# Kernel tuning notes

Measured on AMD Instinct MI355X. Metric: run time of the kernel, lower is better.

Reference implementation:

```python
import jax, jax.numpy as jnp
import numpy as np

EMBED_DIM = 768
NUM_HEADS = 12
HEAD_DIM = EMBED_DIM // NUM_HEADS


def setup_inputs() -> dict:
    key = jax.random.key(0)
    k1, k2, k3, k4, k5 = jax.random.split(key, 5)
    x = jax.random.normal(k1, (2, 4096, EMBED_DIM), dtype=jnp.float32)
    # nn.Linear(embedding_dim, 3*embedding_dim): weight [3d, d], bias [3d]
    w_qkv = jax.random.normal(k2, (3 * EMBED_DIM, EMBED_DIM), dtype=jnp.float32) * (1.0 / np.sqrt(EMBED_DIM))
    b_qkv = jax.random.normal(k3, (3 * EMBED_DIM,), dtype=jnp.float32) * 0.02
    # LayerNorm affine params
    ln_gamma = jnp.ones((EMBED_DIM,), dtype=jnp.float32)
    ln_beta = jnp.zeros((EMBED_DIM,), dtype=jnp.float32)
    return {"x": x, "w_qkv": w_qkv, "b_qkv": b_qkv, "ln_gamma": ln_gamma, "ln_beta": ln_beta}


def _layernorm(x, gamma, beta, eps=1e-5):
    mu = jnp.mean(x, axis=-1, keepdims=True)
    var = jnp.var(x, axis=-1, keepdims=True)
    return (x - mu) * jax.lax.rsqrt(var + eps) * gamma + beta


def reference(x, w_qkv, b_qkv, ln_gamma, ln_beta):
    b, n, d = x.shape
    h, hd = NUM_HEADS, HEAD_DIM
    qkv = x @ w_qkv.T + b_qkv                      # [b, n, 3d]
    qkv = qkv.reshape(b, n, 3, h, hd)
    qkv = jnp.transpose(qkv, (2, 0, 3, 1, 4))      # [3, b, h, n, hd]
    Q, K, V = qkv[0], qkv[1], qkv[2]
    scale = 1.0 / np.sqrt(hd).astype(np.float32)
    scores = jnp.einsum('bhqd,bhkd->bhqk', Q, K) * scale   # [b, h, n, n]
    attn = jax.nn.softmax(scores, axis=-1)
    out = jnp.einsum('bhqk,bhkd->bhqd', attn, V)           # [b, h, n, hd]
    out = jnp.transpose(out, (0, 2, 1, 3)).reshape(b, n, d)
    return _layernorm(x + out, ln_gamma, ln_beta)
```

## Files before the change

kernel.cpp:

```cpp
#include <hip/hip_runtime.h>
#include <stdint.h>

#define NUM_HEADS 12
#define HEAD_DIM 64
#define EMB 768
#define SEQ 4096
#define BATCH 2
#define ROWS (BATCH*SEQ)
#define DQKV (3*EMB)

typedef __attribute__((ext_vector_type(8))) __bf16 bf16x8;
typedef __attribute__((ext_vector_type(4))) float floatx4;

static __device__ __forceinline__ unsigned short f2bf(float f) {
  unsigned int u = __float_as_uint(f);
  u += 0x7FFFu + ((u >> 16) & 1u);
  return (unsigned short)(u >> 16);
}

static __device__ __forceinline__ unsigned int pack_bf2_trunc(float a, float b) {
  return __builtin_amdgcn_perm(__float_as_uint(b), __float_as_uint(a), 0x07060302u);
}

static __device__ __forceinline__ void async_cp16(void* lds, const void* g) {
  __builtin_amdgcn_global_load_lds(
      (__attribute__((address_space(1))) void*)(g),
      (__attribute__((address_space(3))) void*)(lds), 16, 0, 0);
}

__global__ __launch_bounds__(256) void cvt_bf16_kernel(
    const float* __restrict__ src, unsigned short* __restrict__ dst, int n4) {
  int i = blockIdx.x * blockDim.x + threadIdx.x;
  if (i >= n4) return;
  float4 v = ((const float4*)src)[i];
  ushort4 o;
  o.x = f2bf(v.x); o.y = f2bf(v.y); o.z = f2bf(v.z); o.w = f2bf(v.w);
  ((ushort4*)dst)[i] = o;
}

__global__ __launch_bounds__(256) void qkv_gemm_kernel(
    const unsigned short* __restrict__ xb, const unsigned short* __restrict__ wb,
    const float* __restrict__ bias,
    unsigned short* __restrict__ Qb, unsigned short* __restrict__ Kb,
    unsigned short* __restrict__ Vt) {
  __shared__ unsigned short As[128 * 64];
  __shared__ unsigned short Bs[128 * 64];
  const int t = threadIdx.x;
  const int lane = t & 63;
  const int w = t >> 6;
  const int wm = w >> 1, wn = w & 1;
  const int fr = lane & 15, fq = lane >> 4;
  const int fx = fr & 7;
  const int m0 = blockIdx.x * 128;
  const int n0 = blockIdx.y * 128;
  const int lr = t >> 3;
  const int sc = t & 7;

  floatx4 acc[4][4];
#pragma unroll
  for (int i = 0; i < 4; ++i)
#pragma unroll
    for (int j = 0; j < 4; ++j) acc[i][j] = (floatx4)(0.0f);

  for (int k0 = 0; k0 < EMB; k0 += 64) {
    __syncthreads();
#pragma unroll
    for (int i = 0; i < 4; ++i) {
      const int rr = i*32 + lr;
      const int cg = ((sc ^ (lr & 7)) * 8);
      async_cp16(&As[rr*64 + sc*8], &xb[(size_t)(m0 + rr)*EMB + k0 + cg]);
      async_cp16(&Bs[rr*64 + sc*8], &wb[(size_t)(n0 + rr)*EMB + k0 + cg]);
    }
    __syncthreads();
#pragma unroll
    for (int ks = 0; ks < 2; ++ks) {
      bf16x8 af[4], bfr[4];
#pragma unroll
      for (int i = 0; i < 4; ++i)
        af[i] = *(const bf16x8*)&As[(wm*64 + i*16 + fr)*64 + (((ks*4+fq) ^ fx)*8)];
#pragma unroll
      for (int j = 0; j < 4; ++j)
        bfr[j] = *(const bf16x8*)&Bs[(wn*64 + j*16 + fr)*64 + (((ks*4+fq) ^ fx)*8)];
#pragma unroll
      for (int i = 0; i < 4; ++i)
#pragma unroll
        for (int j = 0; j < 4; ++j)
          acc[i][j] = __builtin_amdgcn_mfma_f32_16x16x32_bf16(bfr[j], af[i], acc[i][j], 0, 0, 0);
    }
  }

  const int sel = n0 / EMB;
  const float qscale = 0.125f * 1.4426950408889634f;
  const float sc2 = (sel == 0) ? qscale : 1.0f;
#pragma unroll
  for (int i = 0; i < 4; ++i) {
    const int mr = m0 + wm*64 + i*16 + fr;
    const int b = mr / SEQ;
    const int nn = mr - b*SEQ;
#pragma unroll
    for (int j = 0; j < 4; ++j) {
      const int og = n0 + wn*64 + j*16 + fq*4;
      const int oo = og - sel*EMB;
      const int hh = oo >> 6, dd = oo & 63;
      const float4 bv = *(const float4*)&bias[og];
      if (sel == 2) {
        const size_t vtb = (((size_t)(b*NUM_HEADS + hh))*HEAD_DIM + dd)*SEQ + nn;
        Vt[vtb + 0*SEQ] = f2bf(acc[i][j][0] + bv.x);
        Vt[vtb + 1*SEQ] = f2bf(acc[i][j][1] + bv.y);
        Vt[vtb + 2*SEQ] = f2bf(acc[i][j][2] + bv.z);
        Vt[vtb + 3*SEQ] = f2bf(acc[i][j][3] + bv.w);
      } else {
        unsigned short* dst = (sel == 0) ? Qb : Kb;
        ushort4 pk;
        pk.x = f2bf((acc[i][j][0] + bv.x) * sc2);
        pk.y = f2bf((acc[i][j][1] + bv.y) * sc2);
        pk.z = f2bf((acc[i][j][2] + bv.z) * sc2);
        pk.w = f2bf((acc[i][j][3] + bv.w) * sc2);
        *(ushort4*)&dst[(((size_t)(b*NUM_HEADS + hh))*SEQ + nn)*HEAD_DIM + dd] = pk;
      }
    }
  }
}

__global__ __launch_bounds__(256, 3) void attn_kernel(
    const unsigned short* __restrict__ Qb, const unsigned short* __restrict__ Kb,
    const unsigned short* __restrict__ Vt, unsigned short* __restrict__ Oo) {
  __shared__ unsigned short Ks[128 * 64];
  __shared__ unsigned short Vs[64 * 128];
  const int t = threadIdx.x;
  const int lane = t & 63;
  const int w = t >> 6;
  const int fr = lane & 15, fq = lane >> 4;
  const int fx = fr & 7;
  const int bh = blockIdx.y;
  const int q0 = blockIdx.x * 128 + w * 32;

  bf16x8 aq[2][2];
#pragma unroll
  for (int g = 0; g < 2; ++g) {
    const size_t qoff = ((size_t)bh * SEQ + q0 + g*16 + fr) * HEAD_DIM;
    aq[g][0] = *(const bf16x8*)&Qb[qoff + fq*8];
    aq[g][1] = *(const bf16x8*)&Qb[qoff + 32 + fq*8];
  }

  union { unsigned int u[4]; bf16x8 b; } onesu;
  onesu.u[0] = onesu.u[1] = onesu.u[2] = onesu.u[3] = 0x3F803F80u;
  const bf16x8 onesb = onesu.b;

  floatx4 o[2][4];
  floatx4 lsum[2];
#pragma unroll
  for (int g = 0; g < 2; ++g) {
    lsum[g] = (floatx4)(0.f);
#pragma unroll
    for (int d = 0; d < 4; ++d) o[g][d] = (floatx4)(0.f);
  }

  const size_t kb = (size_t)bh * SEQ * HEAD_DIM;
  const size_t vb = (size_t)bh * HEAD_DIM * SEQ;

  for (int kc = 0; kc < SEQ; kc += 128) {
    __syncthreads();
#pragma unroll
    for (int i = 0; i < 4; ++i) {
      const int chunk = i*256 + t;
      const int r = chunk >> 3, c = chunk & 7;
      async_cp16(&Ks[chunk*8], &Kb[kb + (size_t)(kc + r)*HEAD_DIM + ((c ^ (r&7))*8)]);
    }
#pragma unroll
    for (int i = 0; i < 4; ++i) {
      const int chunk = i*256 + t;
      const int r = chunk >> 4, c = chunk & 15;
      async_cp16(&Vs[chunk*8], &Vt[vb + (size_t)r*SEQ + kc + ((c ^ (r&7))*8)]);
    }
    __syncthreads();

#pragma unroll
    for (int J = 0; J < 4; ++J) {
      floatx4 z[2][2];
#pragma unroll
      for (int jj = 0; jj < 2; ++jj) {
        const int row = (J*2 + jj)*16 + fr;
        bf16x8 k0 = *(const bf16x8*)&Ks[row*64 + ((fq ^ fx)*8)];
        bf16x8 k1 = *(const bf16x8*)&Ks[row*64 + (((fq+4) ^ fx)*8)];
#pragma unroll
        for (int g = 0; g < 2; ++g) {
          floatx4 accz = (floatx4)(0.f);
          accz = __builtin_amdgcn_mfma_f32_16x16x32_bf16(k0, aq[g][0], accz, 0, 0, 0);
          accz = __builtin_amdgcn_mfma_f32_16x16x32_bf16(k1, aq[g][1], accz, 0, 0, 0);
          z[g][jj] = accz;
        }
      }
      bf16x8 ap[2];
#pragma unroll
      for (int g = 0; g < 2; ++g) {
        float e0 = __builtin_amdgcn_exp2f(z[g][0][0]);
        float e1 = __builtin_amdgcn_exp2f(z[g][0][1]);
        float e2 = __builtin_amdgcn_exp2f(z[g][0][2]);
        float e3 = __builtin_amdgcn_exp2f(z[g][0][3]);
        float e4 = __builtin_amdgcn_exp2f(z[g][1][0]);
        float e5 = __builtin_amdgcn_exp2f(z[g][1][1]);
        float e6 = __builtin_amdgcn_exp2f(z[g][1][2]);
        float e7 = __builtin_amdgcn_exp2f(z[g][1][3]);
        union { unsigned int u[4]; bf16x8 b; } cv;
        cv.u[0] = pack_bf2_trunc(e0, e1);
        cv.u[1] = pack_bf2_trunc(e2, e3);
        cv.u[2] = pack_bf2_trunc(e4, e5);
        cv.u[3] = pack_bf2_trunc(e6, e7);
        ap[g] = cv.b;
      }
#pragma unroll
      for (int g = 0; g < 2; ++g)
        lsum[g] = __builtin_amdgcn_mfma_f32_16x16x32_bf16(ap[g], onesb, lsum[g], 0, 0, 0);
#pragma unroll
      for (int dt = 0; dt < 4; ++dt) {
        const int r = dt*16 + fr;
        const int c0 = 4*J + (fq >> 1);
        const int c1 = c0 + 2;
        union { ushort4 h[2]; bf16x8 b; } vv;
        vv.h[0] = *(const ushort4*)&Vs[r*128 + ((c0 ^ fx)*8) + (fq&1)*4];
        vv.h[1] = *(const ushort4*)&Vs[r*128 + ((c1 ^ fx)*8) + (fq&1)*4];
#pragma unroll
        for (int g = 0; g < 2; ++g)
          o[g][dt] = __builtin_amdgcn_mfma_f32_16x16x32_bf16(ap[g], vv.b, o[g][dt], 0, 0, 0);
      }
    }
  }

  const int b = bh / NUM_HEADS, hh = bh - b*NUM_HEADS;
#pragma unroll
  for (int g = 0; g < 2; ++g)
#pragma unroll
    for (int r4 = 0; r4 < 4; ++r4) {
      const float li = 1.0f / lsum[g][r4];
      const size_t obase = ((size_t)b*SEQ + q0 + g*16 + fq*4 + r4)*EMB + hh*HEAD_DIM;
#pragma unroll
      for (int dt = 0; dt < 4; ++dt)
        Oo[obase + dt*16 + fr] = f2bf(o[g][dt][r4] * li);
    }
}

__global__ __launch_bounds__(256) void ln_kernel(
    const float* __restrict__ x, const unsigned short* __restrict__ att,
    const float* __restrict__ gamma, const float* __restrict__ beta,
    float* __restrict__ out) {
  const int row = blockIdx.x;
  const size_t base = (size_t)row * EMB;
  const int t = threadIdx.x;
  float v[3];
  float s = 0.f, s2 = 0.f;
#pragma unroll
  for (int k = 0; k < 3; ++k) {
    const int c = t + k*256;
    float a = __uint_as_float(((unsigned int)att[base + c]) << 16);
    float val = x[base + c] + a;
    v[k] = val; s += val; s2 += val*val;
  }
#pragma unroll
  for (int off = 32; off > 0; off >>= 1) {
    s  += __shfl_down(s,  off);
    s2 += __shfl_down(s2, off);
  }
  __shared__ float red[8];
  if ((t & 63) == 0) { red[t >> 6] = s; red[4 + (t >> 6)] = s2; }
  __syncthreads();
  const float S  = red[0] + red[1] + red[2] + red[3];
  const float S2 = red[4] + red[5] + red[6] + red[7];
  const float mean = S * (1.0f / EMB);
  const float var  = S2 * (1.0f / EMB) - mean * mean;
  const float rstd = rsqrtf(var + 1e-5f);
#pragma unroll
  for (int k = 0; k < 3; ++k) {
    const int c = t + k*256;
    out[base + c] = (v[k] - mean) * rstd * gamma[c] + beta[c];
  }
}

extern "C" void kernel_launch(void* const* d_in, const int* in_sizes, int n_in,
                              void* d_out, int out_size, void* d_ws, size_t ws_size,
                              hipStream_t stream) {
  const float* x      = (const float*)d_in[0];
  const float* w_qkv  = (const float*)d_in[1];
  const float* b_qkv  = (const float*)d_in[2];
  const float* gamma  = (const float*)d_in[3];
  const float* beta   = (const float*)d_in[4];
  float* out = (float*)d_out;

  unsigned short* xb = (unsigned short*)d_ws;
  unsigned short* wb = xb + (size_t)ROWS * EMB;
  unsigned short* Qb = wb + (size_t)DQKV * EMB;
  unsigned short* Kb = Qb + (size_t)ROWS * EMB;
  unsigned short* Vt = Kb + (size_t)ROWS * EMB;
  unsigned short* att = Vt + (size_t)ROWS * EMB;

  cvt_bf16_kernel<<<(ROWS*EMB/4 + 255)/256, 256, 0, stream>>>(x, xb, ROWS*EMB/4);
  cvt_bf16_kernel<<<(DQKV*EMB/4 + 255)/256, 256, 0, stream>>>(w_qkv, wb, DQKV*EMB/4);
  qkv_gemm_kernel<<<dim3(ROWS/128, DQKV/128), 256, 0, stream>>>(xb, wb, b_qkv, Qb, Kb, Vt);
  attn_kernel<<<dim3(SEQ/128, BATCH*NUM_HEADS), 256, 0, stream>>>(Qb, Kb, Vt, att);
  ln_kernel<<<ROWS, 256, 0, stream>>>(x, att, gamma, beta, out);
}
```

Baseline: 258.6 us.

## Split V projection into transposed-output GEMM and widen attention blocks to 8 waves

The QKV GEMM is split into a Q/K kernel and a separate V kernel. The V kernel swaps the MFMA operands so each lane holds four consecutive sequence positions and can write the transposed V with packed 8-byte stores instead of scattered 2-byte stores. The attention kernel now uses 512 threads per block, with each wave handling 16 query rows instead of 32. This halves per-wave register use and the cooperative K/V tile load count per thread, at the cost of each K/V LDS read feeding half as many MFMAs and one extra kernel launch.

New measurement: 286.2 us. 1.11x slower.

```diff
diff --git a/kernel.cpp b/kernel.cpp
--- a/kernel.cpp
+++ b/kernel.cpp
@@ -38,11 +38,10 @@
   ((ushort4*)dst)[i] = o;
 }
 
-__global__ __launch_bounds__(256) void qkv_gemm_kernel(
+__global__ __launch_bounds__(256) void qk_gemm_kernel(
     const unsigned short* __restrict__ xb, const unsigned short* __restrict__ wb,
     const float* __restrict__ bias,
-    unsigned short* __restrict__ Qb, unsigned short* __restrict__ Kb,
-    unsigned short* __restrict__ Vt) {
+    unsigned short* __restrict__ Qb, unsigned short* __restrict__ Kb) {
   __shared__ unsigned short As[128 * 64];
   __shared__ unsigned short Bs[128 * 64];
   const int t = threadIdx.x;
@@ -92,6 +91,7 @@
   const int sel = n0 / EMB;
   const float qscale = 0.125f * 1.4426950408889634f;
   const float sc2 = (sel == 0) ? qscale : 1.0f;
+  unsigned short* dst = (sel == 0) ? Qb : Kb;
 #pragma unroll
   for (int i = 0; i < 4; ++i) {
     const int mr = m0 + wm*64 + i*16 + fr;
@@ -103,26 +103,87 @@
       const int oo = og - sel*EMB;
       const int hh = oo >> 6, dd = oo & 63;
       const float4 bv = *(const float4*)&bias[og];
-      if (sel == 2) {
-        const size_t vtb = (((size_t)(b*NUM_HEADS + hh))*HEAD_DIM + dd)*SEQ + nn;
-        Vt[vtb + 0*SEQ] = f2bf(acc[i][j][0] + bv.x);
-        Vt[vtb + 1*SEQ] = f2bf(acc[i][j][1] + bv.y);
-        Vt[vtb + 2*SEQ] = f2bf(acc[i][j][2] + bv.z);
-        Vt[vtb + 3*SEQ] = f2bf(acc[i][j][3] + bv.w);
-      } else {
-        unsigned short* dst = (sel == 0) ? Qb : Kb;
-        ushort4 pk;
-        pk.x = f2bf((acc[i][j][0] + bv.x) * sc2);
-        pk.y = f2bf((acc[i][j][1] + bv.y) * sc2);
-        pk.z = f2bf((acc[i][j][2] + bv.z) * sc2);
-        pk.w = f2bf((acc[i][j][3] + bv.w) * sc2);
-        *(ushort4*)&dst[(((size_t)(b*NUM_HEADS + hh))*SEQ + nn)*HEAD_DIM + dd] = pk;
-      }
-    }
-  }
-}
-
-__global__ __launch_bounds__(256, 3) void attn_kernel(
+      ushort4 pk;
+      pk.x = f2bf((acc[i][j][0] + bv.x) * sc2);
+      pk.y = f2bf((acc[i][j][1] + bv.y) * sc2);
+      pk.z = f2bf((acc[i][j][2] + bv.z) * sc2);
+      pk.w = f2bf((acc[i][j][3] + bv.w) * sc2);
+      *(ushort4*)&dst[(((size_t)(b*NUM_HEADS + hh))*SEQ + nn)*HEAD_DIM + dd] = pk;
+    }
+  }
+}
+
+__global__ __launch_bounds__(256) void v_gemm_kernel(
+    const unsigned short* __restrict__ xb, const unsigned short* __restrict__ wb,
+    const float* __restrict__ bias, unsigned short* __restrict__ Vt) {
+  __shared__ unsigned short As[128 * 64];
+  __shared__ unsigned short Bs[128 * 64];
+  const int t = threadIdx.x;
+  const int lane = t & 63;
+  const int w = t >> 6;
+  const int wm = w >> 1, wn = w & 1;
+  const int fr = lane & 15, fq = lane >> 4;
+  const int fx = fr & 7;
+  const int m0 = blockIdx.x * 128;
+  const int n0 = 2*EMB + blockIdx.y * 128;
+  const int lr = t >> 3;
+  const int sc = t & 7;
+
+  floatx4 acc[4][4];
+#pragma unroll
+  for (int i = 0; i < 4; ++i)
+#pragma unroll
+    for (int j = 0; j < 4; ++j) acc[i][j] = (floatx4)(0.0f);
+
+  for (int k0 = 0; k0 < EMB; k0 += 64) {
+    __syncthreads();
+#pragma unroll
+    for (int i = 0; i < 4; ++i) {
+      const int rr = i*32 + lr;
+      const int cg = ((sc ^ (lr & 7)) * 8);
+      async_cp16(&As[rr*64 + sc*8], &xb[(size_t)(m0 + rr)*EMB + k0 + cg]);
+      async_cp16(&Bs[rr*64 + sc*8], &wb[(size_t)(n0 + rr)*EMB + k0 + cg]);
+    }
+    __syncthreads();
+#pragma unroll
+    for (int ks = 0; ks < 2; ++ks) {
+      bf16x8 af[4], bfr[4];
+#pragma unroll
+      for (int i = 0; i < 4; ++i)
+        af[i] = *(const bf16x8*)&As[(wm*64 + i*16 + fr)*64 + (((ks*4+fq) ^ fx)*8)];
+#pragma unroll
+      for (int j = 0; j < 4; ++j)
+        bfr[j] = *(const bf16x8*)&Bs[(wn*64 + j*16 + fr)*64 + (((ks*4+fq) ^ fx)*8)];
+#pragma unroll
+      for (int i = 0; i < 4; ++i)
+#pragma unroll
+        for (int j = 0; j < 4; ++j)
+          acc[i][j] = __builtin_amdgcn_mfma_f32_16x16x32_bf16(af[i], bfr[j], acc[i][j], 0, 0, 0);
+    }
+  }
+
+#pragma unroll
+  for (int i = 0; i < 4; ++i) {
+    const int mr = m0 + wm*64 + i*16 + fq*4;
+    const int b = mr / SEQ;
+    const int nn = mr - b*SEQ;
+#pragma unroll
+    for (int j = 0; j < 4; ++j) {
+      const int feat = n0 + wn*64 + j*16 + fr;
+      const int oo = feat - 2*EMB;
+      const int hh = oo >> 6, dd = oo & 63;
+      const float bv = bias[feat];
+      ushort4 pk;
+      pk.x = f2bf(acc[i][j][0] + bv);
+      pk.y = f2bf(acc[i][j][1] + bv);
+      pk.z = f2bf(acc[i][j][2] + bv);
+      pk.w = f2bf(acc[i][j][3] + bv);
+      *(ushort4*)&Vt[(((size_t)(b*NUM_HEADS + hh))*HEAD_DIM + dd)*SEQ + nn] = pk;
+    }
+  }
+}
+
+__global__ __launch_bounds__(512, 6) void attn_kernel(
     const unsigned short* __restrict__ Qb, const unsigned short* __restrict__ Kb,
     const unsigned short* __restrict__ Vt, unsigned short* __restrict__ Oo) {
   __shared__ unsigned short Ks[128 * 64];
@@ -133,28 +194,20 @@
   const int fr = lane & 15, fq = lane >> 4;
   const int fx = fr & 7;
   const int bh = blockIdx.y;
-  const int q0 = blockIdx.x * 128 + w * 32;
-
-  bf16x8 aq[2][2];
-#pragma unroll
-  for (int g = 0; g < 2; ++g) {
-    const size_t qoff = ((size_t)bh * SEQ + q0 + g*16 + fr) * HEAD_DIM;
-    aq[g][0] = *(const bf16x8*)&Qb[qoff + fq*8];
-    aq[g][1] = *(const bf16x8*)&Qb[qoff + 32 + fq*8];
-  }
+  const int q0 = blockIdx.x * 128 + w * 16;
+
+  const size_t qoff = ((size_t)bh * SEQ + q0 + fr) * HEAD_DIM;
+  bf16x8 aq0 = *(const bf16x8*)&Qb[qoff + fq*8];
+  bf16x8 aq1 = *(const bf16x8*)&Qb[qoff + 32 + fq*8];
 
   union { unsigned int u[4]; bf16x8 b; } onesu;
   onesu.u[0] = onesu.u[1] = onesu.u[2] = onesu.u[3] = 0x3F803F80u;
   const bf16x8 onesb = onesu.b;
 
-  floatx4 o[2][4];
-  floatx4 lsum[2];
-#pragma unroll
-  for (int g = 0; g < 2; ++g) {
-    lsum[g] = (floatx4)(0.f);
-#pragma unroll
-    for (int d = 0; d < 4; ++d) o[g][d] = (floatx4)(0.f);
-  }
+  floatx4 o[4];
+  floatx4 lsum = (floatx4)(0.f);
+#pragma unroll
+  for (int d = 0; d < 4; ++d) o[d] = (floatx4)(0.f);
 
   const size_t kb = (size_t)bh * SEQ * HEAD_DIM;
   const size_t vb = (size_t)bh * HEAD_DIM * SEQ;
@@ -162,14 +215,14 @@
   for (int kc = 0; kc < SEQ; kc += 128) {
     __syncthreads();
 #pragma unroll
-    for (int i = 0; i < 4; ++i) {
-      const int chunk = i*256 + t;
+    for (int i = 0; i < 2; ++i) {
+      const int chunk = i*512 + t;
       const int r = chunk >> 3, c = chunk & 7;
       async_cp16(&Ks[chunk*8], &Kb[kb + (size_t)(kc + r)*HEAD_DIM + ((c ^ (r&7))*8)]);
     }
 #pragma unroll
-    for (int i = 0; i < 4; ++i) {
-      const int chunk = i*256 + t;
+    for (int i = 0; i < 2; ++i) {
+      const int chunk = i*512 + t;
       const int r = chunk >> 4, c = chunk & 15;
       async_cp16(&Vs[chunk*8], &Vt[vb + (size_t)r*SEQ + kc + ((c ^ (r&7))*8)]);
     }
@@ -177,41 +230,32 @@
 
 #pragma unroll
     for (int J = 0; J < 4; ++J) {
-      floatx4 z[2][2];
+      floatx4 z[2];
 #pragma unroll
       for (int jj = 0; jj < 2; ++jj) {
         const int row = (J*2 + jj)*16 + fr;
         bf16x8 k0 = *(const bf16x8*)&Ks[row*64 + ((fq ^ fx)*8)];
         bf16x8 k1 = *(const bf16x8*)&Ks[row*64 + (((fq+4) ^ fx)*8)];
-#pragma unroll
-        for (int g = 0; g < 2; ++g) {
-          floatx4 accz = (floatx4)(0.f);
-          accz = __builtin_amdgcn_mfma_f32_16x16x32_bf16(k0, aq[g][0], accz, 0, 0, 0);
-          accz = __builtin_amdgcn_mfma_f32_16x16x32_bf16(k1, aq[g][1], accz, 0, 0, 0);
-          z[g][jj] = accz;
-        }
+        floatx4 accz = (floatx4)(0.f);
+        accz = __builtin_amdgcn_mfma_f32_16x16x32_bf16(k0, aq0, accz, 0, 0, 0);
+        accz = __builtin_amdgcn_mfma_f32_16x16x32_bf16(k1, aq1, accz, 0, 0, 0);
+        z[jj] = accz;
       }
-      bf16x8 ap[2];
-#pragma unroll
-      for (int g = 0; g < 2; ++g) {
-        float e0 = __builtin_amdgcn_exp2f(z[g][0][0]);
-        float e1 = __builtin_amdgcn_exp2f(z[g][0][1]);
-        float e2 = __builtin_amdgcn_exp2f(z[g][0][2]);
-        float e3 = __builtin_amdgcn_exp2f(z[g][0][3]);
-        float e4 = __builtin_amdgcn_exp2f(z[g][1][0]);
-        float e5 = __builtin_amdgcn_exp2f(z[g][1][1]);
-        float e6 = __builtin_amdgcn_exp2f(z[g][1][2]);
-        float e7 = __builtin_amdgcn_exp2f(z[g][1][3]);
-        union { unsigned int u[4]; bf16x8 b; } cv;
-        cv.u[0] = pack_bf2_trunc(e0, e1);
-        cv.u[1] = pack_bf2_trunc(e2, e3);
-        cv.u[2] = pack_bf2_trunc(e4, e5);
-        cv.u[3] = pack_bf2_trunc(e6, e7);
-        ap[g] = cv.b;
-      }
-#pragma unroll
-      for (int g = 0; g < 2; ++g)
-        lsum[g] = __builtin_amdgcn_mfma_f32_16x16x32_bf16(ap[g], onesb, lsum[g], 0, 0, 0);
+      float e0 = __builtin_amdgcn_exp2f(z[0][0]);
+      float e1 = __builtin_amdgcn_exp2f(z[0][1]);
+      float e2 = __builtin_amdgcn_exp2f(z[0][2]);
+      float e3 = __builtin_amdgcn_exp2f(z[0][3]);
+      float e4 = __builtin_amdgcn_exp2f(z[1][0]);
+      float e5 = __builtin_amdgcn_exp2f(z[1][1]);
+      float e6 = __builtin_amdgcn_exp2f(z[1][2]);
+      float e7 = __builtin_amdgcn_exp2f(z[1][3]);
+      union { unsigned int u[4]; bf16x8 b; } cv;
+      cv.u[0] = pack_bf2_trunc(e0, e1);
+      cv.u[1] = pack_bf2_trunc(e2, e3);
+      cv.u[2] = pack_bf2_trunc(e4, e5);
+      cv.u[3] = pack_bf2_trunc(e6, e7);
+      const bf16x8 ap = cv.b;
+      lsum = __builtin_amdgcn_mfma_f32_16x16x32_bf16(ap, onesb, lsum, 0, 0, 0);
 #pragma unroll
       for (int dt = 0; dt < 4; ++dt) {
         const int r = dt*16 + fr;
@@ -220,24 +264,20 @@
         union { ushort4 h[2]; bf16x8 b; } vv;
         vv.h[0] = *(const ushort4*)&Vs[r*128 + ((c0 ^ fx)*8) + (fq&1)*4];
         vv.h[1] = *(const ushort4*)&Vs[r*128 + ((c1 ^ fx)*8) + (fq&1)*4];
-#pragma unroll
-        for (int g = 0; g < 2; ++g)
-          o[g][dt] = __builtin_amdgcn_mfma_f32_16x16x32_bf16(ap[g], vv.b, o[g][dt], 0, 0, 0);
+        o[dt] = __builtin_amdgcn_mfma_f32_16x16x32_bf16(ap, vv.b, o[dt], 0, 0, 0);
       }
     }
   }
 
   const int b = bh / NUM_HEADS, hh = bh - b*NUM_HEADS;
 #pragma unroll
-  for (int g = 0; g < 2; ++g)
-#pragma unroll
-    for (int r4 = 0; r4 < 4; ++r4) {
-      const float li = 1.0f / lsum[g][r4];
-      const size_t obase = ((size_t)b*SEQ + q0 + g*16 + fq*4 + r4)*EMB + hh*HEAD_DIM;
-#pragma unroll
-      for (int dt = 0; dt < 4; ++dt)
-        Oo[obase + dt*16 + fr] = f2bf(o[g][dt][r4] * li);
-    }
+  for (int r4 = 0; r4 < 4; ++r4) {
+    const float li = 1.0f / lsum[r4];
+    const size_t obase = ((size_t)b*SEQ + q0 + fq*4 + r4)*EMB + hh*HEAD_DIM;
+#pragma unroll
+    for (int dt = 0; dt < 4; ++dt)
+      Oo[obase + dt*16 + fr] = f2bf(o[dt][r4] * li);
+  }
 }
 
 __global__ __launch_bounds__(256) void ln_kernel(
@@ -295,7 +335,8 @@
 
   cvt_bf16_kernel<<<(ROWS*EMB/4 + 255)/256, 256, 0, stream>>>(x, xb, ROWS*EMB/4);
   cvt_bf16_kernel<<<(DQKV*EMB/4 + 255)/256, 256, 0, stream>>>(w_qkv, wb, DQKV*EMB/4);
-  qkv_gemm_kernel<<<dim3(ROWS/128, DQKV/128), 256, 0, stream>>>(xb, wb, b_qkv, Qb, Kb, Vt);
-  attn_kernel<<<dim3(SEQ/128, BATCH*NUM_HEADS), 256, 0, stream>>>(Qb, Kb, Vt, att);
+  qk_gemm_kernel<<<dim3(ROWS/128, 2*EMB/128), 256, 0, stream>>>(xb, wb, b_qkv, Qb, Kb);
+  v_gemm_kernel<<<dim3(ROWS/128, EMB/128), 256, 0, stream>>>(xb, wb, b_qkv, Vt);
+  attn_kernel<<<dim3(SEQ/128, BATCH*NUM_HEADS), 512, 0, stream>>>(Qb, Kb, Vt, att);
   ln_kernel<<<ROWS, 256, 0, stream>>>(x, att, gamma, beta, out);
 }
```

## Split V projection into its own GEMM with permuted transposed layout for vector loads

Applied to the files above, without the earlier changes.

Splits the QKV GEMM into a Q/K kernel and a separate V kernel. The V kernel swaps the MFMA operand order so each lane holds four consecutive sequence positions, and it writes V-transposed with a permuted key order as packed 4-element stores instead of scattered 2-byte stores. With that permutation the attention kernel can fetch V fragments with one 16-byte LDS read instead of two 8-byte reads. It also raises the attention kernel's occupancy hint from 3 to 5 blocks per CU, which may cause register spills.

New measurement: 295.1 us. +14.1%, slower.

```diff
diff --git a/kernel.cpp b/kernel.cpp
--- a/kernel.cpp
+++ b/kernel.cpp
@@ -26,6 +26,10 @@
   __builtin_amdgcn_global_load_lds(
       (__attribute__((address_space(1))) void*)(g),
       (__attribute__((address_space(3))) void*)(lds), 16, 0, 0);
+}
+
+static __device__ __forceinline__ int perm_key(int nn) {
+  return (nn & ~31) | (((nn >> 2) & 3) * 8 + ((nn >> 4) & 1) * 4 + (nn & 3));
 }
 
 __global__ __launch_bounds__(256) void cvt_bf16_kernel(
@@ -38,11 +42,10 @@
   ((ushort4*)dst)[i] = o;
 }
 
-__global__ __launch_bounds__(256) void qkv_gemm_kernel(
+__global__ __launch_bounds__(256) void qk_gemm_kernel(
     const unsigned short* __restrict__ xb, const unsigned short* __restrict__ wb,
     const float* __restrict__ bias,
-    unsigned short* __restrict__ Qb, unsigned short* __restrict__ Kb,
-    unsigned short* __restrict__ Vt) {
+    unsigned short* __restrict__ Qb, unsigned short* __restrict__ Kb) {
   __shared__ unsigned short As[128 * 64];
   __shared__ unsigned short Bs[128 * 64];
   const int t = threadIdx.x;
@@ -92,6 +95,7 @@
   const int sel = n0 / EMB;
   const float qscale = 0.125f * 1.4426950408889634f;
   const float sc2 = (sel == 0) ? qscale : 1.0f;
+  unsigned short* dst = (sel == 0) ? Qb : Kb;
 #pragma unroll
   for (int i = 0; i < 4; ++i) {
     const int mr = m0 + wm*64 + i*16 + fr;
@@ -103,26 +107,87 @@
       const int oo = og - sel*EMB;
       const int hh = oo >> 6, dd = oo & 63;
       const float4 bv = *(const float4*)&bias[og];
-      if (sel == 2) {
-        const size_t vtb = (((size_t)(b*NUM_HEADS + hh))*HEAD_DIM + dd)*SEQ + nn;
-        Vt[vtb + 0*SEQ] = f2bf(acc[i][j][0] + bv.x);
-        Vt[vtb + 1*SEQ] = f2bf(acc[i][j][1] + bv.y);
-        Vt[vtb + 2*SEQ] = f2bf(acc[i][j][2] + bv.z);
-        Vt[vtb + 3*SEQ] = f2bf(acc[i][j][3] + bv.w);
-      } else {
-        unsigned short* dst = (sel == 0) ? Qb : Kb;
-        ushort4 pk;
-        pk.x = f2bf((acc[i][j][0] + bv.x) * sc2);
-        pk.y = f2bf((acc[i][j][1] + bv.y) * sc2);
-        pk.z = f2bf((acc[i][j][2] + bv.z) * sc2);
-        pk.w = f2bf((acc[i][j][3] + bv.w) * sc2);
-        *(ushort4*)&dst[(((size_t)(b*NUM_HEADS + hh))*SEQ + nn)*HEAD_DIM + dd] = pk;
-      }
-    }
-  }
-}
-
-__global__ __launch_bounds__(256, 3) void attn_kernel(
+      ushort4 pk;
+      pk.x = f2bf((acc[i][j][0] + bv.x) * sc2);
+      pk.y = f2bf((acc[i][j][1] + bv.y) * sc2);
+      pk.z = f2bf((acc[i][j][2] + bv.z) * sc2);
+      pk.w = f2bf((acc[i][j][3] + bv.w) * sc2);
+      *(ushort4*)&dst[(((size_t)(b*NUM_HEADS + hh))*SEQ + nn)*HEAD_DIM + dd] = pk;
+    }
+  }
+}
+
+__global__ __launch_bounds__(256) void v_gemm_kernel(
+    const unsigned short* __restrict__ xb, const unsigned short* __restrict__ wb,
+    const float* __restrict__ bias, unsigned short* __restrict__ Vt) {
+  __shared__ unsigned short As[128 * 64];
+  __shared__ unsigned short Bs[128 * 64];
+  const int t = threadIdx.x;
+  const int lane = t & 63;
+  const int w = t >> 6;
+  const int wm = w >> 1, wn = w & 1;
+  const int fr = lane & 15, fq = lane >> 4;
+  const int fx = fr & 7;
+  const int m0 = blockIdx.x * 128;
+  const int n0 = 2*EMB + blockIdx.y * 128;
+  const int lr = t >> 3;
+  const int sc = t & 7;
+
+  floatx4 acc[4][4];
+#pragma unroll
+  for (int i = 0; i < 4; ++i)
+#pragma unroll
+    for (int j = 0; j < 4; ++j) acc[i][j] = (floatx4)(0.0f);
+
+  for (int k0 = 0; k0 < EMB; k0 += 64) {
+    __syncthreads();
+#pragma unroll
+    for (int i = 0; i < 4; ++i) {
+      const int rr = i*32 + lr;
+      const int cg = ((sc ^ (lr & 7)) * 8);
+      async_cp16(&As[rr*64 + sc*8], &xb[(size_t)(m0 + rr)*EMB + k0 + cg]);
+      async_cp16(&Bs[rr*64 + sc*8], &wb[(size_t)(n0 + rr)*EMB + k0 + cg]);
+    }
+    __syncthreads();
+#pragma unroll
+    for (int ks = 0; ks < 2; ++ks) {
+      bf16x8 af[4], bfr[4];
+#pragma unroll
+      for (int i = 0; i < 4; ++i)
+        af[i] = *(const bf16x8*)&As[(wm*64 + i*16 + fr)*64 + (((ks*4+fq) ^ fx)*8)];
+#pragma unroll
+      for (int j = 0; j < 4; ++j)
+        bfr[j] = *(const bf16x8*)&Bs[(wn*64 + j*16 + fr)*64 + (((ks*4+fq) ^ fx)*8)];
+#pragma unroll
+      for (int i = 0; i < 4; ++i)
+#pragma unroll
+        for (int j = 0; j < 4; ++j)
+          acc[i][j] = __builtin_amdgcn_mfma_f32_16x16x32_bf16(af[i], bfr[j], acc[i][j], 0, 0, 0);
+    }
+  }
+
+#pragma unroll
+  for (int i = 0; i < 4; ++i) {
+    const int mr = m0 + wm*64 + i*16 + fq*4;
+    const int b = mr / SEQ;
+    const int nn = perm_key(mr - b*SEQ);
+#pragma unroll
+    for (int j = 0; j < 4; ++j) {
+      const int feat = n0 + wn*64 + j*16 + fr;
+      const int oo = feat - 2*EMB;
+      const int hh = oo >> 6, dd = oo & 63;
+      const float bv = bias[feat];
+      ushort4 pk;
+      pk.x = f2bf(acc[i][j][0] + bv);
+      pk.y = f2bf(acc[i][j][1] + bv);
+      pk.z = f2bf(acc[i][j][2] + bv);
+      pk.w = f2bf(acc[i][j][3] + bv);
+      *(ushort4*)&Vt[(((size_t)(b*NUM_HEADS + hh))*HEAD_DIM + dd)*SEQ + nn] = pk;
+    }
+  }
+}
+
+__global__ __launch_bounds__(256, 5) void attn_kernel(
     const unsigned short* __restrict__ Qb, const unsigned short* __restrict__ Kb,
     const unsigned short* __restrict__ Vt, unsigned short* __restrict__ Oo) {
   __shared__ unsigned short Ks[128 * 64];
@@ -215,14 +280,10 @@
 #pragma unroll
       for (int dt = 0; dt < 4; ++dt) {
         const int r = dt*16 + fr;
-        const int c0 = 4*J + (fq >> 1);
-        const int c1 = c0 + 2;
-        union { ushort4 h[2]; bf16x8 b; } vv;
-        vv.h[0] = *(const ushort4*)&Vs[r*128 + ((c0 ^ fx)*8) + (fq&1)*4];
-        vv.h[1] = *(const ushort4*)&Vs[r*128 + ((c1 ^ fx)*8) + (fq&1)*4];
+        const bf16x8 vvb = *(const bf16x8*)&Vs[r*128 + (((4*J + fq) ^ fx)*8)];
 #pragma unroll
         for (int g = 0; g < 2; ++g)
-          o[g][dt] = __builtin_amdgcn_mfma_f32_16x16x32_bf16(ap[g], vv.b, o[g][dt], 0, 0, 0);
+          o[g][dt] = __builtin_amdgcn_mfma_f32_16x16x32_bf16(ap[g], vvb, o[g][dt], 0, 0, 0);
       }
     }
   }
@@ -295,7 +356,8 @@
 
   cvt_bf16_kernel<<<(ROWS*EMB/4 + 255)/256, 256, 0, stream>>>(x, xb, ROWS*EMB/4);
   cvt_bf16_kernel<<<(DQKV*EMB/4 + 255)/256, 256, 0, stream>>>(w_qkv, wb, DQKV*EMB/4);
-  qkv_gemm_kernel<<<dim3(ROWS/128, DQKV/128), 256, 0, stream>>>(xb, wb, b_qkv, Qb, Kb, Vt);
+  qk_gemm_kernel<<<dim3(ROWS/128, 2*EMB/128), 256, 0, stream>>>(xb, wb, b_qkv, Qb, Kb);
+  v_gemm_kernel<<<dim3(ROWS/128, EMB/128), 256, 0, stream>>>(xb, wb, b_qkv, Vt);
   attn_kernel<<<dim3(SEQ/128, BATCH*NUM_HEADS), 256, 0, stream>>>(Qb, Kb, Vt, att);
   ln_kernel<<<ROWS, 256, 0, stream>>>(x, att, gamma, beta, out);
 }
```
